# Performance work log

Measured on AMD Instinct MI355X. Metric: run time of the kernel, lower is better.

## Reference

```python
import jax, jax.numpy as jnp
import numpy as np
from jax import lax

TAU = 2.0
EPS = 1e-5
STEP = 10      # time steps
RATIO = 4     # TIM_ratio
HEADS = 16
SCALE = 0.25


@jax.custom_vjp
def _spike(v):
    return (v > 0.0).astype(v.dtype)

def _spike_fwd(v):
    return _spike(v), v

def _spike_bwd(v, g):
    alpha = 4.0  # sigmoid surrogate gradient
    s = jax.nn.sigmoid(alpha * v)
    return (g * alpha * s * (1.0 - s),)

_spike.defvjp(_spike_fwd, _spike_bwd)


def lif(x, vth=1.0):
    """LIF neuron over leading time dim: mem += (x-mem)/tau, fire, hard reset (detached)."""
    def step(mem, xt):
        mem = mem + (xt - mem) / TAU
        s = _spike(mem - vth)
        mem = mem * (1.0 - lax.stop_gradient(s))
        return mem, s
    _, out = lax.scan(step, jnp.zeros_like(x[0]), x)
    return out


def bn(x, p, axis):
    """Inference-mode batchnorm; p = stacked (gamma, beta, mean, var) along dim 0."""
    g, b, m, v = p
    sh = [1] * x.ndim
    sh[axis] = -1
    return (x - m.reshape(sh)) / jnp.sqrt(v.reshape(sh) + EPS) * g.reshape(sh) + b.reshape(sh)


def conv3d(x, w, groups=1):
    return lax.conv_general_dilated(
        x, w, window_strides=(1, 1, 1), padding=[(1, 1)] * 3,
        dimension_numbers=('NCDHW', 'OIDHW', 'NCDHW'),
        feature_group_count=groups)


def tim(x, up_w, bn1, down_w, bn2):
    # x: (T, B, C, H, W); conv3d treats T as channels, (C,H,W) as the volume
    T, B, C, H, W = x.shape
    y = conv3d(jnp.swapaxes(x, 0, 1), up_w)                      # (B, T*R, C, H, W)
    y = jnp.swapaxes(bn(y, bn1, 1), 0, 1)                        # (T*R, B, C, H, W)
    # MyNode reshapes (T*R*B, ...) into STEP time chunks of size R*B
    y = lif(y.reshape(STEP, -1, C, H, W)).reshape(T * RATIO, B, C, H, W)
    y = conv3d(jnp.swapaxes(y, 0, 1), down_w, groups=STEP)       # (B, T, C, H, W)
    y = jnp.swapaxes(bn(y, bn2, 1), 0, 1)                        # (T, B, C, H, W)
    return lif(y)


def ssa(x, q_w, q_bn, k_w, k_bn, v_w, v_bn, proj_w, proj_bn,
        tim_up_w, tim_bn1, tim_down_w, tim_bn2):
    T, B, C, H, W = x.shape
    N = H * W
    d = C // HEADS
    xf = x.reshape(T * B, C, N)

    def branch(w, bnp):
        y = bn(jnp.einsum('oc,bcn->bon', w, xf), bnp, 1).reshape(T, B, C, H, W)
        y = tim(y, tim_up_w, tim_bn1, tim_down_w, tim_bn2)       # binary spikes
        y = y.reshape(T, B, C, N).transpose(0, 1, 3, 2)          # (T, B, N, C)
        return y.reshape(T, B, N, HEADS, d).transpose(0, 1, 3, 2, 4)  # (T, B, h, N, d)

    q = branch(q_w, q_bn)
    k = branch(k_w, k_bn)
    v = branch(v_w, v_bn)
    attn = jnp.einsum('tbhnd,tbhmd->tbhnm', q, k)                # no softmax (spiking attn)
    o = jnp.einsum('tbhnm,tbhmd->tbhnd', attn, v) * SCALE
    o = o.transpose(0, 1, 2, 4, 3).reshape(T, B, C, N)           # merge (h, d) -> C
    o = lif(o, vth=0.5)                                          # attn_lif, threshold 0.5
    o = bn(jnp.einsum('oc,tbcn->tbon', proj_w, o), proj_bn, 2)   # 1x1 conv1d + BN1d
    return lif(o).reshape(T, B, C, H, W)


def mlp(x, fc1_w, fc1_b, fc1_bn, fc2_w, fc2_b, fc2_bn):
    T, B, C, H, W = x.shape
    y = jnp.einsum('oc,tbchw->tbohw', fc1_w, x) + fc1_b.reshape(1, 1, -1, 1, 1)
    y = lif(bn(y, fc1_bn, 2))
    y = jnp.einsum('oc,tbchw->tbohw', fc2_w, y) + fc2_b.reshape(1, 1, -1, 1, 1)
    return lif(bn(y, fc2_bn, 2))


def setup_inputs() -> dict:
    key = jax.random.key(0)
    ks = jax.random.split(key, 24)
    T, B, C, H, W = 10, 4, 256, 16, 16
    HID = 1024

    def bnp(k, c):
        k1, k2, k3, k4 = jax.random.split(k, 4)
        gamma = jax.random.uniform(k1, (c,), minval=0.5, maxval=1.5)
        beta = 0.1 * jax.random.normal(k2, (c,))
        mean = 0.1 * jax.random.normal(k3, (c,))
        var = jax.random.uniform(k4, (c,), minval=0.5, maxval=1.5)
        return jnp.stack([gamma, beta, mean, var]).astype(jnp.float32)

    inp = {
        'x': jax.random.normal(ks[0], (T, B, C, H, W), jnp.float32),
        'q_w': jax.random.normal(ks[1], (C, C)) / np.sqrt(C),
        'q_bn': bnp(ks[2], C),
        'k_w': jax.random.normal(ks[3], (C, C)) / np.sqrt(C),
        'k_bn': bnp(ks[4], C),
        'v_w': jax.random.normal(ks[5], (C, C)) / np.sqrt(C),
        'v_bn': bnp(ks[6], C),
        'proj_w': jax.random.normal(ks[7], (C, C)) / np.sqrt(C),
        'proj_bn': bnp(ks[8], C),
        'tim_up_w': jax.random.normal(ks[9], (STEP * RATIO, STEP, 3, 3, 3)) / np.sqrt(STEP * 27),
        'tim_bn1': bnp(ks[10], STEP * RATIO),
        'tim_down_w': jax.random.normal(ks[11], (STEP, RATIO, 3, 3, 3)) / np.sqrt(RATIO * 27),
        'tim_bn2': bnp(ks[12], STEP),
        'fc1_w': jax.random.normal(ks[13], (HID, C)) / np.sqrt(C),
        'fc1_b': 0.1 * jax.random.normal(ks[14], (HID,)),
        'fc1_bn': bnp(ks[15], HID),
        'fc2_w': jax.random.normal(ks[16], (C, HID)) / np.sqrt(HID),
        'fc2_b': 0.1 * jax.random.normal(ks[17], (C,)),
        'fc2_bn': bnp(ks[18], C),
    }
    return {k: v.astype(jnp.float32) for k, v in inp.items()}


def reference(x, q_w, q_bn, k_w, k_bn, v_w, v_bn, proj_w, proj_bn,
              tim_up_w, tim_bn1, tim_down_w, tim_bn2,
              fc1_w, fc1_b, fc1_bn, fc2_w, fc2_b, fc2_bn):
    h = x + ssa(x, q_w, q_bn, k_w, k_bn, v_w, v_bn, proj_w, proj_bn,
                tim_up_w, tim_bn1, tim_down_w, tim_bn2)
    return h + mlp(h, fc1_w, fc1_b, fc1_bn, fc2_w, fc2_b, fc2_bn)
```

## Files before the change

### kernel.cpp

```cpp
#include <hip/hip_runtime.h>
#include <cstdint>
#include <cstddef>

#define EPSF 1e-5f

typedef __attribute__((ext_vector_type(8))) short short8;
typedef __attribute__((ext_vector_type(4))) float f32x4;

__device__ __forceinline__ unsigned short bf16_rne(float f) {
    unsigned int u = __float_as_uint(f);
    u += 0x7FFFu + ((u >> 16) & 1u);
    return (unsigned short)(u >> 16);
}
__device__ __forceinline__ float bf16f(unsigned short h) {
    return __uint_as_float(((unsigned int)h) << 16);
}

__device__ __forceinline__ void split_pack_body(
    const float* __restrict__ W, unsigned short* __restrict__ P,
    int O, int K, int idx)
{
    const int OT = O >> 4, KT = K >> 5;
    const int lane = idx & 63, tile = idx >> 6;
    const int kt = tile % KT, ot = tile / KT;
    const int quad = lane >> 4, l15 = lane & 15;
    const int row = ot * 16 + l15, col = kt * 32 + quad * 8;
    const size_t base = ((size_t)ot * KT + kt) * 512 + lane * 8;
    const size_t sOff = (size_t)OT * KT * 512;
#pragma unroll
    for (int j = 0; j < 8; ++j) {
        float v = W[(size_t)row * K + col + j];
        unsigned short h1 = bf16_rne(v);
        float r = v - bf16f(h1);
        unsigned short h2 = bf16_rne(r);
        float r2 = r - bf16f(h2);
        P[base + j] = h1;
        P[sOff + base + j] = h2;
        P[2 * sOff + base + j] = bf16_rne(r2);
    }
}

__global__ __launch_bounds__(256) void split_pack_k(
    const float* __restrict__ W, unsigned short* __restrict__ P, int O, int K)
{
    int idx = blockIdx.x * 256 + threadIdx.x;
    if (idx >= (O * K) >> 3) return;
    split_pack_body(W, P, O, K, idx);
}

struct SplitArgs { const float* W[3]; unsigned short* P[3]; };
__global__ __launch_bounds__(256) void split_pack3_k(SplitArgs sa, int O, int K)
{
    int idx = blockIdx.x * 256 + threadIdx.x;
    if (idx >= (O * K) >> 3) return;
    split_pack_body(sa.W[blockIdx.y], sa.P[blockIdx.y], O, K, idx);
}

__global__ __launch_bounds__(256) void bpack_k(
    const float* __restrict__ B, unsigned short* __restrict__ BP,
    int K, int N, int S)
{
    const int KT = K >> 5, NT16 = N >> 4;
    int idx = blockIdx.x * 256 + threadIdx.x;
    if (idx >= S * NT16 * KT * 64) return;
    const int lane = idx & 63;
    int tile = idx >> 6;
    const int kt = tile % KT; tile /= KT;
    const int n16 = tile % NT16; const int s = tile / NT16;
    const int quad = lane >> 4, l15 = lane & 15;
    const size_t base = (size_t)idx * 8;
    const size_t sOff = (size_t)S * NT16 * KT * 512;
    const float* src = B + (size_t)s * K * N + (size_t)(kt * 32 + quad * 8) * N
                         + n16 * 16 + l15;
#pragma unroll
    for (int j = 0; j < 8; ++j) {
        float v = src[(size_t)j * N];
        unsigned short h1 = bf16_rne(v);
        float r = v - bf16f(h1);
        unsigned short h2 = bf16_rne(r);
        float r2 = r - bf16f(h2);
        BP[base + j] = h1;
        BP[sOff + base + j] = h2;
        BP[2 * sOff + base + j] = bf16_rne(r2);
    }
}

struct MArgs { const unsigned short* W[3]; float* Out[3]; const float* bn[3]; };

#define MM(AP, BQ)                                                            \
    {                                                                         \
        _Pragma("unroll") for (int mt = 0; mt < 2; ++mt)                      \
        _Pragma("unroll") for (int nt = 0; nt < 2; ++nt)                      \
            acc[mt][nt] = __builtin_amdgcn_mfma_f32_16x16x32_bf16(            \
                Af[AP][mt], Bf[BQ][nt], acc[mt][nt], 0, 0, 0);                \
    }

__global__ __launch_bounds__(256, 4) void mfma_gemm3(
    MArgs a, const unsigned short* __restrict__ BP,
    const float* __restrict__ bias, int O, int K, int N, int nB)
{
    const unsigned short* __restrict__ W = a.W[blockIdx.z];
    float* __restrict__ Out = a.Out[blockIdx.z];
    const float* __restrict__ bnp = a.bn[blockIdx.z];
    const int OT = O >> 4, KT = K >> 5, NT16 = N >> 4;
    const size_t sA = (size_t)OT * KT * 512;
    const size_t sB = (size_t)gridDim.y * NT16 * KT * 512;

    const int slice  = blockIdx.y;
    const int tilesn = N >> 6;
    const int to = (blockIdx.x / tilesn) << 6;
    const int tn = (blockIdx.x % tilesn) << 6;
    const int tid = threadIdx.x;
    const int wid = tid >> 6, lane = tid & 63;
    const int quad = lane >> 4, l15 = lane & 15;
    const int wm = (wid >> 1) << 5, wn = (wid & 1) << 5;
    const int oti0 = (to + wm) >> 4;
    const int n160 = (tn + wn) >> 4;

    f32x4 acc[2][2];
#pragma unroll
    for (int mt = 0; mt < 2; ++mt)
#pragma unroll
        for (int nt = 0; nt < 2; ++nt)
#pragma unroll
            for (int r = 0; r < 4; ++r) acc[mt][nt][r] = 0.0f;

    for (int kt = 0; kt < KT; ++kt) {
        short8 Af[3][2], Bf[3][2];
#pragma unroll
        for (int mt = 0; mt < 2; ++mt) {
            const size_t fa = ((size_t)(oti0 + mt) * KT + kt) * 512 + lane * 8;
            Af[0][mt] = *(const short8*)(W + fa);
            Af[1][mt] = *(const short8*)(W + sA + fa);
            Af[2][mt] = *(const short8*)(W + 2 * sA + fa);
        }
#pragma unroll
        for (int nt = 0; nt < 2; ++nt) {
            const size_t fb =
                (((size_t)slice * NT16 + n160 + nt) * KT + kt) * 512 + lane * 8;
            Bf[0][nt] = *(const short8*)(BP + fb);
            if (nB == 3) {
                Bf[1][nt] = *(const short8*)(BP + sB + fb);
                Bf[2][nt] = *(const short8*)(BP + 2 * sB + fb);
            }
        }
        if (nB == 3) {
            MM(0, 0) MM(0, 1) MM(1, 0) MM(0, 2) MM(1, 1) MM(2, 0)
        } else {
            MM(0, 0) MM(1, 0) MM(2, 0)
        }
    }

    float* Op = Out + (size_t)slice * O * N;
#pragma unroll
    for (int mt = 0; mt < 2; ++mt) {
#pragma unroll
        for (int r = 0; r < 4; ++r) {
            const int o = to + wm + (mt << 4) + (quad << 2) + r;
            float g = bnp[o], bb = bnp[O + o], m = bnp[2 * O + o], vv = bnp[3 * O + o];
            float sq = sqrtf(vv + EPSF);
            float bs = bias ? bias[o] : 0.0f;
#pragma unroll
            for (int nt = 0; nt < 2; ++nt) {
                const int n = tn + wn + (nt << 4) + l15;
                float val = acc[mt][nt][r] + bs;
                Op[(size_t)o * N + n] = (val - m) / sq * g + bb;
            }
        }
    }
}

__global__ __launch_bounds__(256) void wt_k(
    const float* __restrict__ up_w, float* __restrict__ WT)
{
    int idx = blockIdx.x * 256 + threadIdx.x;
    if (idx >= 12960) return;
    int slot = idx % 48, tq = idx / 48;
    int g = slot / 12, u = slot % 12;
    float v = 0.0f;
    if (u < 10) v = up_w[(4 * u + g) * 270 + tq];
    WT[idx] = v;
}

struct TimArgs { const float* Y[3]; };

__global__ __launch_bounds__(256, 8) void tim_up5(
    TimArgs ta, const float* __restrict__ WT,
    const float* __restrict__ bn1, unsigned char* __restrict__ USPK)
{
    __shared__ float smem[5 * 3 * 200];
    const float* __restrict__ Y = ta.Y[blockIdx.z];
    unsigned char* __restrict__ SPK = USPK + (size_t)blockIdx.z * 10485760;
    const int c = blockIdx.x;
    const int b = blockIdx.y >> 1, half = blockIdx.y & 1;
    const int tid = threadIdx.x;
    const int lane = tid & 63;
    const int g = __builtin_amdgcn_readfirstlane(tid >> 6);
    const int hb2 = (lane >> 4) << 1;
    const int wc = lane & 15;

    float acc[2][10];
#pragma unroll
    for (int i = 0; i < 2; ++i)
#pragma unroll
        for (int u = 0; u < 10; ++u) acc[i][u] = 0.0f;

#pragma unroll 1
    for (int ph = 0; ph < 2; ++ph) {
        __syncthreads();
        for (int idx = tid; idx < 3000; idx += 256) {
            int t = ph * 5 + idx / 600, rem = idx % 600;
            int cc = rem / 200, p = rem % 200;
            int rr = p / 20, col = p % 20;
            int h = half * 8 + rr - 1, ww = col - 1;
            int cs = c + cc - 1;
            float v = 0.0f;
            if (cs >= 0 && cs < 256 && h >= 0 && h < 16 && ww >= 0 && ww < 16)
                v = Y[((t * 4 + b) * 256 + cs) * 256 + h * 16 + ww];
            smem[idx] = v;
        }
        __syncthreads();

#pragma unroll 1
        for (int tt = 0; tt < 5; ++tt) {
            const int t = ph * 5 + tt;
#pragma unroll
            for (int kd = 0; kd < 3; ++kd) {
                const float* sp = &smem[tt * 600 + kd * 200 + hb2 * 20 + wc];
                float vr[4][3];
#pragma unroll
                for (int r = 0; r < 4; ++r)
#pragma unroll
                    for (int kc = 0; kc < 3; ++kc)
                        vr[r][kc] = sp[r * 20 + kc];
#pragma unroll
                for (int q = 0; q < 9; ++q) {
                    const int kh = q / 3, kw = q % 3;
                    const float4* wp =
                        (const float4*)&WT[(t * 27 + kd * 9 + q) * 48 + g * 12];
                    float4 w0 = wp[0], w1 = wp[1];
                    float4 w2 = wp[2];
                    float wr[10] = {w0.x, w0.y, w0.z, w0.w, w1.x,
                                    w1.y, w1.z, w1.w, w2.x, w2.y};
#pragma unroll
                    for (int u = 0; u < 10; ++u)
#pragma unroll
                        for (int i = 0; i < 2; ++i)
                            acc[i][u] = fmaf(wr[u], vr[i + kh][kw], acc[i][u]);
                }
            }
        }
    }

#pragma unroll
    for (int i = 0; i < 2; ++i) {
        const int h = half * 8 + hb2 + i;
        float mem = 0.0f;
#pragma unroll
        for (int s = 0; s < 10; ++s) {
            const int uc = 4 * s + g;
            float ga = bn1[uc], be = bn1[40 + uc], mu = bn1[80 + uc], va = bn1[120 + uc];
            float xv = (acc[i][s] - mu) / sqrtf(va + EPSF) * ga + be;
            mem += (xv - mem) * 0.5f;
            unsigned char spk = mem > 1.0f ? 1 : 0;
            SPK[(((size_t)b * 40 + uc) * 256 + c) * 256 + h * 16 + wc] = spk;
            mem = spk ? 0.0f : mem;
        }
    }
}

struct PtrArgs { float* p[3]; };
struct CPtrArgs { const float* p[3]; };

__global__ __launch_bounds__(256) void tim_down_pre5(
    const unsigned char* __restrict__ USPK, const float* __restrict__ w,
    const float* __restrict__ bn2, PtrArgs PY)
{
    __shared__ float smem[4 * 3 * 324];
    const int br = blockIdx.z / 10, t = blockIdx.z % 10;
    const unsigned char* __restrict__ SPK = USPK + (size_t)br * 10485760;
    float* __restrict__ PreY = PY.p[br];
    const int c = blockIdx.x, b = blockIdx.y;
    const int tid = threadIdx.x;
    for (int idx = tid; idx < 3888; idx += 256) {
        int r = idx / 972, rem = idx % 972;
        int cc = rem / 324, p = rem % 324;
        int hh = p / 18 - 1, ww = p % 18 - 1;
        int cs = c + cc - 1;
        float v = 0.0f;
        if (cs >= 0 && cs < 256 && hh >= 0 && hh < 16 && ww >= 0 && ww < 16)
            v = (float)SPK[(((size_t)b * 40 + 4 * t + r) * 256 + cs) * 256 + hh * 16 + ww];
        smem[idx] = v;
    }
    __syncthreads();
    const int h = tid >> 4, wq = tid & 15;
    float a = 0.0f;
#pragma unroll
    for (int r = 0; r < 4; ++r)
#pragma unroll
        for (int kd = 0; kd < 3; ++kd) {
            const float* wp = w + ((t * 4 + r) * 3 + kd) * 9;
#pragma unroll
            for (int kh = 0; kh < 3; ++kh)
#pragma unroll
                for (int kw = 0; kw < 3; ++kw)
                    a = fmaf(wp[kh * 3 + kw],
                             smem[r * 972 + kd * 324 + (h + kh) * 18 + (wq + kw)], a);
        }
    a = (a - bn2[20 + t]) / sqrtf(bn2[30 + t] + EPSF) * bn2[t] + bn2[10 + t];
    PreY[((t * 4 + b) * 256 + c) * 256 + tid] = a;
}

__global__ __launch_bounds__(256) void lif_down3(CPtrArgs PY, PtrArgs SB)
{
    const float* __restrict__ PreY = PY.p[blockIdx.y];
    float* __restrict__ S = SB.p[blockIdx.y];
    const int idx = blockIdx.x * 256 + threadIdx.x;
    float mem = 0.0f;
    for (int t = 0; t < 10; ++t) {
        float v = PreY[t * 262144 + idx];
        mem += (v - mem) * 0.5f;
        float spk = mem > 1.0f ? 1.0f : 0.0f;
        S[t * 262144 + idx] = spk;
        mem = spk > 0.0f ? 0.0f : mem;
    }
}

__global__ __launch_bounds__(256) void ktv_k(
    const float* __restrict__ SK, const float* __restrict__ SV,
    float* __restrict__ KTV)
{
    __shared__ float ks[16 * 257], vs[16 * 257];
    const int bi = blockIdx.x;
    const int t = bi >> 6, b = (bi >> 4) & 3, hd = bi & 15;
    const int tid = threadIdx.x;
    for (int i = tid; i < 4096; i += 256) {
        int row = i >> 8, col = i & 255;
        ks[row * 257 + col] = SK[((t * 4 + b) * 256 + hd * 16 + row) * 256 + col];
        vs[row * 257 + col] = SV[((t * 4 + b) * 256 + hd * 16 + row) * 256 + col];
    }
    __syncthreads();
    const int j = tid >> 4, j2 = tid & 15;
    float a0 = 0.0f, a1 = 0.0f, a2 = 0.0f, a3 = 0.0f;
#pragma unroll 4
    for (int n = 0; n < 256; n += 4) {
        a0 = fmaf(ks[j * 257 + n + 0], vs[j2 * 257 + n + 0], a0);
        a1 = fmaf(ks[j * 257 + n + 1], vs[j2 * 257 + n + 1], a1);
        a2 = fmaf(ks[j * 257 + n + 2], vs[j2 * 257 + n + 2], a2);
        a3 = fmaf(ks[j * 257 + n + 3], vs[j2 * 257 + n + 3], a3);
    }
    KTV[((t * 4 + b) * 16 + hd) * 256 + tid] = (a0 + a1) + (a2 + a3);
}

__global__ __launch_bounds__(256) void attn_k2(
    const float* __restrict__ SQ, const float* __restrict__ KTV,
    unsigned short* __restrict__ PSPK)
{
    __shared__ float kt[2560];
    __shared__ float qs[16 * 17];
    const int x = blockIdx.x;
    const int b = x >> 8, hd = (x >> 4) & 15, ng = x & 15;
    const int tid = threadIdx.x;
    const int j2 = tid >> 4, nl = tid & 15;
    const int n = ng * 16 + nl;
    for (int i = tid; i < 2560; i += 256) {
        int t = i >> 8;
        kt[i] = KTV[((t * 4 + b) * 16 + hd) * 256 + (i & 255)];
    }
    const int c = hd * 16 + j2;
    const int ktile = c >> 5, quad = (c >> 3) & 3, jj = c & 7;
    const int lane = quad * 16 + nl;
    float mem = 0.0f;
    for (int t = 0; t < 10; ++t) {
        __syncthreads();
        qs[nl * 17 + j2] = SQ[((t * 4 + b) * 256 + hd * 16 + j2) * 256 + n];
        __syncthreads();
        float a = 0.0f;
#pragma unroll
        for (int j = 0; j < 16; ++j)
            a = fmaf(qs[nl * 17 + j], kt[t * 256 + j * 16 + j2], a);
        a *= 0.25f;
        mem += (a - mem) * 0.5f;
        float spk = mem > 0.5f ? 1.0f : 0.0f;
        PSPK[((((size_t)(t * 4 + b) * 16 + ng) * 8 + ktile) * 512) + lane * 8 + jj] =
            spk > 0.0f ? (unsigned short)0x3F80 : (unsigned short)0;
        mem = spk > 0.0f ? 0.0f : mem;
    }
}

__global__ __launch_bounds__(256) void ssa_lif_res(
    const float* __restrict__ P, const float* __restrict__ x,
    float* __restrict__ H)
{
    const int idx = blockIdx.x * 256 + threadIdx.x;
    float mem = 0.0f;
    for (int t = 0; t < 10; ++t) {
        float v = P[t * 262144 + idx];
        mem += (v - mem) * 0.5f;
        float spk = mem > 1.0f ? 1.0f : 0.0f;
        H[t * 262144 + idx] = x[t * 262144 + idx] + spk;
        mem = spk > 0.0f ? 0.0f : mem;
    }
}

__global__ __launch_bounds__(256) void lif_pack(
    const float* __restrict__ A, unsigned short* __restrict__ PB)
{
    const int idx = blockIdx.x * 256 + threadIdx.x;
    const int b = idx >> 18, rem = idx & 262143;
    const int hid = rem >> 8, hw = rem & 255;
    const int ktile = hid >> 5, quad = (hid >> 3) & 3, jj = hid & 7;
    const int n16 = hw >> 4, l15 = hw & 15;
    const int lane = quad * 16 + l15;
    float mem = 0.0f;
    for (int t = 0; t < 10; ++t) {
        float v = A[t * 1048576 + idx];
        mem += (v - mem) * 0.5f;
        float spk = mem > 1.0f ? 1.0f : 0.0f;
        PB[((((size_t)(t * 4 + b) * 16 + n16) * 32 + ktile) * 512) + lane * 8 + jj] =
            spk > 0.0f ? (unsigned short)0x3F80 : (unsigned short)0;
        mem = spk > 0.0f ? 0.0f : mem;
    }
}

__global__ __launch_bounds__(256) void final_k(
    const float* __restrict__ P, const float* __restrict__ H,
    float* __restrict__ out)
{
    const int idx = blockIdx.x * 256 + threadIdx.x;
    float mem = 0.0f;
    for (int t = 0; t < 10; ++t) {
        float v = P[t * 262144 + idx];
        mem += (v - mem) * 0.5f;
        float spk = mem > 1.0f ? 1.0f : 0.0f;
        out[t * 262144 + idx] = H[t * 262144 + idx] + spk;
        mem = spk > 0.0f ? 0.0f : mem;
    }
}

extern "C" void kernel_launch(void* const* d_in, const int* in_sizes, int n_in,
                              void* d_out, int out_size, void* d_ws, size_t ws_size,
                              hipStream_t stream)
{
    const float* x        = (const float*)d_in[0];
    const float* q_w      = (const float*)d_in[1];
    const float* q_bn     = (const float*)d_in[2];
    const float* k_w      = (const float*)d_in[3];
    const float* k_bn     = (const float*)d_in[4];
    const float* v_w      = (const float*)d_in[5];
    const float* v_bn     = (const float*)d_in[6];
    const float* proj_w   = (const float*)d_in[7];
    const float* proj_bn  = (const float*)d_in[8];
    const float* up_w     = (const float*)d_in[9];
    const float* bn1      = (const float*)d_in[10];
    const float* down_w   = (const float*)d_in[11];
    const float* bn2      = (const float*)d_in[12];
    const float* fc1_w    = (const float*)d_in[13];
    const float* fc1_b    = (const float*)d_in[14];
    const float* fc1_bn   = (const float*)d_in[15];
    const float* fc2_w    = (const float*)d_in[16];
    const float* fc2_b    = (const float*)d_in[17];
    const float* fc2_bn   = (const float*)d_in[18];

    float* ws   = (float*)d_ws;
    float* Y    = ws;
    float* ASPK = Y + 2621440;
    float* SQ   = ASPK + 10485760;
    float* SK   = SQ + 2621440;
    float* SV   = SK + 2621440;
    float* KTV  = SV + 2621440;
    float* WT   = KTV;

    unsigned short* qs_s = (unsigned short*)ASPK;
    unsigned short* ks_s = qs_s + 196608;
    unsigned short* vs_s = qs_s + 393216;
    unsigned short* xp_s = qs_s + 589824;

    wt_k<<<51, 256, 0, stream>>>(up_w, WT);
    SplitArgs sa;
    sa.W[0] = q_w; sa.W[1] = k_w; sa.W[2] = v_w;
    sa.P[0] = qs_s; sa.P[1] = ks_s; sa.P[2] = vs_s;
    split_pack3_k<<<dim3(32, 3), 256, 0, stream>>>(sa, 256, 256);
    bpack_k<<<1280, 256, 0, stream>>>(x, xp_s, 256, 256, 40);

    MArgs qkv;
    qkv.W[0] = qs_s;  qkv.W[1] = ks_s;  qkv.W[2] = vs_s;
    qkv.Out[0] = Y; qkv.Out[1] = SK; qkv.Out[2] = SV;
    qkv.bn[0] = q_bn; qkv.bn[1] = k_bn; qkv.bn[2] = v_bn;
    mfma_gemm3<<<dim3(16, 40, 3), 256, 0, stream>>>(qkv, xp_s, nullptr, 256, 256, 256, 3);

    unsigned char* USPK = (unsigned char*)ASPK;
    TimArgs ta; ta.Y[0] = Y; ta.Y[1] = SK; ta.Y[2] = SV;
    tim_up5<<<dim3(256, 8, 3), 256, 0, stream>>>(ta, WT, bn1, USPK);

    PtrArgs PY; PY.p[0] = Y; PY.p[1] = SK; PY.p[2] = SV;
    tim_down_pre5<<<dim3(256, 4, 30), 256, 0, stream>>>(USPK, down_w, bn2, PY);

    CPtrArgs PYc; PYc.p[0] = Y; PYc.p[1] = SK; PYc.p[2] = SV;
    PtrArgs SB; SB.p[0] = SQ; SB.p[1] = SK; SB.p[2] = SV;
    lif_down3<<<dim3(1024, 3), 256, 0, stream>>>(PYc, SB);

    ktv_k<<<640, 256, 0, stream>>>(SK, SV, KTV);
    unsigned short* PSPK = (unsigned short*)Y;
    attn_k2<<<1024, 256, 0, stream>>>(SQ, KTV, PSPK);

    unsigned short* pj_s = (unsigned short*)ASPK;
    split_pack_k<<<32, 256, 0, stream>>>(proj_w, pj_s, 256, 256);
    MArgs gp; gp.W[0] = gp.W[1] = gp.W[2] = pj_s;
    gp.Out[0] = gp.Out[1] = gp.Out[2] = SQ;
    gp.bn[0] = gp.bn[1] = gp.bn[2] = proj_bn;
    mfma_gemm3<<<dim3(16, 40, 1), 256, 0, stream>>>(gp, PSPK, nullptr, 256, 256, 256, 1);
    ssa_lif_res<<<1024, 256, 0, stream>>>(SQ, x, SV);

    unsigned short* f1b = (unsigned short*)SQ;
    bpack_k<<<1280, 256, 0, stream>>>(SV, f1b, 256, 256, 40);
    unsigned short* f1_s = (unsigned short*)Y;
    split_pack_k<<<128, 256, 0, stream>>>(fc1_w, f1_s, 1024, 256);
    MArgs g1; g1.W[0] = g1.W[1] = g1.W[2] = f1_s;
    g1.Out[0] = g1.Out[1] = g1.Out[2] = ASPK;
    g1.bn[0] = g1.bn[1] = g1.bn[2] = fc1_bn;
    mfma_gemm3<<<dim3(64, 40, 1), 256, 0, stream>>>(g1, f1b, fc1_b, 1024, 256, 256, 3);

    unsigned short* PB2 = (unsigned short*)SQ;
    lif_pack<<<4096, 256, 0, stream>>>(ASPK, PB2);
    unsigned short* f2_s = (unsigned short*)Y;
    split_pack_k<<<128, 256, 0, stream>>>(fc2_w, f2_s, 256, 1024);
    MArgs g2; g2.W[0] = g2.W[1] = g2.W[2] = f2_s;
    g2.Out[0] = g2.Out[1] = g2.Out[2] = ASPK;
    g2.bn[0] = g2.bn[1] = g2.bn[2] = fc2_bn;
    mfma_gemm3<<<dim3(16, 40, 1), 256, 0, stream>>>(g2, PB2, fc2_b, 256, 1024, 256, 1);
    final_k<<<1024, 256, 0, stream>>>(ASPK, SV, (float*)d_out);
}
```

Measured before the change: 682.5 us.

## Move TIM up-conv from scalar FMA to split-bf16 MFMA with LDS transpose

Replaces the scalar-FP32 tim_up kernel with an MFMA version. The 3D-conv taps become the K dimension (27 padded to 32), the 40 up-channels become M, and pixels become N. Weights and activations are split into three bf16 parts, and six cross-product MFMAs keep near-FP32 accuracy. Accumulators go through LDS so the LIF epilogue can run one pixel per thread, and each block now covers a full 16x16 plane. The cost is the per-element split conversion on the activation side, a larger LDS footprint with lower occupancy, and the six-fold MFMA work.

```diff
diff --git a/kernel.cpp b/kernel.cpp
--- a/kernel.cpp
+++ b/kernel.cpp
@@ -170,50 +170,74 @@
     }
 }
 
-__global__ __launch_bounds__(256) void wt_k(
-    const float* __restrict__ up_w, float* __restrict__ WT)
+__global__ __launch_bounds__(256) void wpack6_k(
+    const float* __restrict__ up_w, unsigned short* __restrict__ AP)
 {
     int idx = blockIdx.x * 256 + threadIdx.x;
-    if (idx >= 12960) return;
-    int slot = idx % 48, tq = idx / 48;
-    int g = slot / 12, u = slot % 12;
-    float v = 0.0f;
-    if (u < 10) v = up_w[(4 * u + g) * 270 + tq];
-    WT[idx] = v;
+    if (idx >= 1920) return;
+    const int lane = idx & 63, rest = idx >> 6;
+    const int t = rest % 10, mt = rest / 10;
+    const int quad = lane >> 4, l15 = lane & 15;
+    const int uc = mt * 16 + l15;
+    const size_t base = ((size_t)mt * 10 + t) * 512 + lane * 8;
+#pragma unroll
+    for (int j = 0; j < 8; ++j) {
+        int tap = quad * 8 + j;
+        float v = 0.0f;
+        if (uc < 40 && tap < 27) v = up_w[uc * 270 + t * 27 + tap];
+        unsigned short h1 = bf16_rne(v);
+        float r = v - bf16f(h1);
+        unsigned short h2 = bf16_rne(r);
+        float r2 = r - bf16f(h2);
+        AP[base + j] = h1;
+        AP[15360 + base + j] = h2;
+        AP[30720 + base + j] = bf16_rne(r2);
+    }
 }
 
 struct TimArgs { const float* Y[3]; };
 
-__global__ __launch_bounds__(256, 8) void tim_up5(
-    TimArgs ta, const float* __restrict__ WT,
+__global__ __launch_bounds__(256, 2) void tim_up6(
+    TimArgs ta, const unsigned short* __restrict__ AP,
     const float* __restrict__ bn1, unsigned char* __restrict__ USPK)
 {
-    __shared__ float smem[5 * 3 * 200];
+    __shared__ float smem[12336];
     const float* __restrict__ Y = ta.Y[blockIdx.z];
     unsigned char* __restrict__ SPK = USPK + (size_t)blockIdx.z * 10485760;
-    const int c = blockIdx.x;
-    const int b = blockIdx.y >> 1, half = blockIdx.y & 1;
+    const int c = blockIdx.x, b = blockIdx.y;
     const int tid = threadIdx.x;
-    const int lane = tid & 63;
-    const int g = __builtin_amdgcn_readfirstlane(tid >> 6);
-    const int hb2 = (lane >> 4) << 1;
-    const int wc = lane & 15;
-
-    float acc[2][10];
-#pragma unroll
-    for (int i = 0; i < 2; ++i)
-#pragma unroll
-        for (int u = 0; u < 10; ++u) acc[i][u] = 0.0f;
+    const int wid = tid >> 6, lane = tid & 63;
+    const int quad = lane >> 4, l15 = lane & 15;
+
+    int offs[8];
+#pragma unroll
+    for (int j = 0; j < 8; ++j) {
+        int tap = quad * 8 + j;
+        if (tap < 27) {
+            int kd = tap / 9, rem = tap - kd * 9;
+            int kh = rem / 3, kw = rem - kh * 3;
+            offs[j] = kd * 360 + kh * 20 + kw;
+        } else offs[j] = 0;
+    }
+
+    f32x4 acc[3][4];
+#pragma unroll
+    for (int mt = 0; mt < 3; ++mt)
+#pragma unroll
+        for (int ng = 0; ng < 4; ++ng)
+#pragma unroll
+            for (int r = 0; r < 4; ++r) acc[mt][ng][r] = 0.0f;
 
 #pragma unroll 1
     for (int ph = 0; ph < 2; ++ph) {
         __syncthreads();
-        for (int idx = tid; idx < 3000; idx += 256) {
-            int t = ph * 5 + idx / 600, rem = idx % 600;
-            int cc = rem / 200, p = rem % 200;
-            int rr = p / 20, col = p % 20;
-            int h = half * 8 + rr - 1, ww = col - 1;
-            int cs = c + cc - 1;
+        for (int idx = tid; idx < 5400; idx += 256) {
+            int tt = idx / 1080, rem = idx % 1080;
+            int kd = rem / 360, p = rem % 360;
+            int row = p / 20, col = p % 20;
+            int t = ph * 5 + tt;
+            int h = row - 1, ww = col - 1;
+            int cs = c + kd - 1;
             float v = 0.0f;
             if (cs >= 0 && cs < 256 && h >= 0 && h < 16 && ww >= 0 && ww < 16)
                 v = Y[((t * 4 + b) * 256 + cs) * 256 + h * 16 + ww];
@@ -224,46 +248,73 @@
 #pragma unroll 1
         for (int tt = 0; tt < 5; ++tt) {
             const int t = ph * 5 + tt;
-#pragma unroll
-            for (int kd = 0; kd < 3; ++kd) {
-                const float* sp = &smem[tt * 600 + kd * 200 + hb2 * 20 + wc];
-                float vr[4][3];
-#pragma unroll
-                for (int r = 0; r < 4; ++r)
-#pragma unroll
-                    for (int kc = 0; kc < 3; ++kc)
-                        vr[r][kc] = sp[r * 20 + kc];
-#pragma unroll
-                for (int q = 0; q < 9; ++q) {
-                    const int kh = q / 3, kw = q % 3;
-                    const float4* wp =
-                        (const float4*)&WT[(t * 27 + kd * 9 + q) * 48 + g * 12];
-                    float4 w0 = wp[0], w1 = wp[1];
-                    float4 w2 = wp[2];
-                    float wr[10] = {w0.x, w0.y, w0.z, w0.w, w1.x,
-                                    w1.y, w1.z, w1.w, w2.x, w2.y};
-#pragma unroll
-                    for (int u = 0; u < 10; ++u)
-#pragma unroll
-                        for (int i = 0; i < 2; ++i)
-                            acc[i][u] = fmaf(wr[u], vr[i + kh][kw], acc[i][u]);
+            short8 Af[3][3];
+#pragma unroll
+            for (int mt = 0; mt < 3; ++mt) {
+                const size_t fa = ((size_t)mt * 10 + t) * 512 + lane * 8;
+                Af[0][mt] = *(const short8*)(AP + fa);
+                Af[1][mt] = *(const short8*)(AP + 15360 + fa);
+                Af[2][mt] = *(const short8*)(AP + 30720 + fa);
+            }
+#pragma unroll
+            for (int ng = 0; ng < 4; ++ng) {
+                const int base = tt * 1080 + (wid * 4 + ng) * 20 + l15;
+                short8 Bf0, Bf1, Bf2;
+#pragma unroll
+                for (int j = 0; j < 8; ++j) {
+                    float v = smem[base + offs[j]];
+                    unsigned short h1 = bf16_rne(v);
+                    float r = v - bf16f(h1);
+                    unsigned short h2 = bf16_rne(r);
+                    float r2 = r - bf16f(h2);
+                    Bf0[j] = (short)h1;
+                    Bf1[j] = (short)h2;
+                    Bf2[j] = (short)bf16_rne(r2);
+                }
+#pragma unroll
+                for (int mt = 0; mt < 3; ++mt) {
+                    acc[mt][ng] = __builtin_amdgcn_mfma_f32_16x16x32_bf16(
+                        Af[0][mt], Bf0, acc[mt][ng], 0, 0, 0);
+                    acc[mt][ng] = __builtin_amdgcn_mfma_f32_16x16x32_bf16(
+                        Af[0][mt], Bf1, acc[mt][ng], 0, 0, 0);
+                    acc[mt][ng] = __builtin_amdgcn_mfma_f32_16x16x32_bf16(
+                        Af[1][mt], Bf0, acc[mt][ng], 0, 0, 0);
+                    acc[mt][ng] = __builtin_amdgcn_mfma_f32_16x16x32_bf16(
+                        Af[0][mt], Bf2, acc[mt][ng], 0, 0, 0);
+                    acc[mt][ng] = __builtin_amdgcn_mfma_f32_16x16x32_bf16(
+                        Af[1][mt], Bf1, acc[mt][ng], 0, 0, 0);
+                    acc[mt][ng] = __builtin_amdgcn_mfma_f32_16x16x32_bf16(
+                        Af[2][mt], Bf0, acc[mt][ng], 0, 0, 0);
                 }
             }
         }
     }
 
-#pragma unroll
-    for (int i = 0; i < 2; ++i) {
-        const int h = half * 8 + hb2 + i;
+    __syncthreads();
+#pragma unroll
+    for (int mt = 0; mt < 3; ++mt)
+#pragma unroll
+        for (int ng = 0; ng < 4; ++ng)
+#pragma unroll
+            for (int r = 0; r < 4; ++r) {
+                const int uc = mt * 16 + quad * 4 + r;
+                const int pix = (wid * 4 + ng) * 16 + l15;
+                smem[uc * 257 + pix] = acc[mt][ng][r];
+            }
+    __syncthreads();
+
+    const int pix = tid;
+#pragma unroll
+    for (int g = 0; g < 4; ++g) {
         float mem = 0.0f;
 #pragma unroll
         for (int s = 0; s < 10; ++s) {
             const int uc = 4 * s + g;
             float ga = bn1[uc], be = bn1[40 + uc], mu = bn1[80 + uc], va = bn1[120 + uc];
-            float xv = (acc[i][s] - mu) / sqrtf(va + EPSF) * ga + be;
+            float xv = (smem[uc * 257 + pix] - mu) / sqrtf(va + EPSF) * ga + be;
             mem += (xv - mem) * 0.5f;
             unsigned char spk = mem > 1.0f ? 1 : 0;
-            SPK[(((size_t)b * 40 + uc) * 256 + c) * 256 + h * 16 + wc] = spk;
+            SPK[(((size_t)b * 40 + uc) * 256 + c) * 256 + pix] = spk;
             mem = spk ? 0.0f : mem;
         }
     }
@@ -469,14 +520,14 @@
     float* SK   = SQ + 2621440;
     float* SV   = SK + 2621440;
     float* KTV  = SV + 2621440;
-    float* WT   = KTV;
+    unsigned short* AP = (unsigned short*)KTV;
 
     unsigned short* qs_s = (unsigned short*)ASPK;
     unsigned short* ks_s = qs_s + 196608;
     unsigned short* vs_s = qs_s + 393216;
     unsigned short* xp_s = qs_s + 589824;
 
-    wt_k<<<51, 256, 0, stream>>>(up_w, WT);
+    wpack6_k<<<8, 256, 0, stream>>>(up_w, AP);
     SplitArgs sa;
     sa.W[0] = q_w; sa.W[1] = k_w; sa.W[2] = v_w;
     sa.P[0] = qs_s; sa.P[1] = ks_s; sa.P[2] = vs_s;
@@ -491,7 +542,7 @@
 
     unsigned char* USPK = (unsigned char*)ASPK;
     TimArgs ta; ta.Y[0] = Y; ta.Y[1] = SK; ta.Y[2] = SV;
-    tim_up5<<<dim3(256, 8, 3), 256, 0, stream>>>(ta, WT, bn1, USPK);
+    tim_up6<<<dim3(256, 4, 3), 256, 0, stream>>>(ta, AP, bn1, USPK);
 
     PtrArgs PY; PY.p[0] = Y; PY.p[1] = SK; PY.p[2] = SV;
     tim_down_pre5<<<dim3(256, 4, 30), 256, 0, stream>>>(USPK, down_w, bn2, PY);
```

New measurement: 673.0 us. About the same (-1.4%).
